# Kernel optimization log

Measured on AMD Instinct MI355X. Metric: run time of the kernel, lower is better.

## Reference

```python
import jax, jax.numpy as jnp
import numpy as np

D_MODEL, D_STATE, D_CONV, EXPAND = 1024, 16, 4, 2
D_INNER = D_MODEL * EXPAND
BATCH, SEQ = 2, 2048


def setup_inputs() -> dict:
    key = jax.random.key(0)
    ks = jax.random.split(key, 10)
    s = lambda d: 1.0 / np.sqrt(d)
    return {
        "x": jax.random.normal(ks[0], (BATCH, SEQ, D_MODEL), jnp.float32),
        "norm_w": jnp.ones((D_MODEL,), jnp.float32),
        "norm_b": jnp.zeros((D_MODEL,), jnp.float32),
        "W_in": jax.random.normal(ks[1], (2 * D_INNER, D_MODEL), jnp.float32) * s(D_MODEL),
        "conv_w": jax.random.normal(ks[2], (D_INNER, D_CONV), jnp.float32) * s(D_CONV),
        "conv_b": jnp.zeros((D_INNER,), jnp.float32),
        "W_dt": jax.random.normal(ks[3], (D_INNER, D_INNER), jnp.float32) * s(D_INNER),
        "b_dt": jnp.zeros((D_INNER,), jnp.float32),
        "W_B": jax.random.normal(ks[4], (D_STATE, D_INNER), jnp.float32) * s(D_INNER),
        "W_C": jax.random.normal(ks[5], (D_STATE, D_INNER), jnp.float32) * s(D_INNER),
        "D": jnp.ones((D_INNER,), jnp.float32),
        "A_log": jnp.broadcast_to(jnp.log(jnp.arange(1, D_STATE + 1, dtype=jnp.float32)), (D_INNER, D_STATE)),
        "W_out": jax.random.normal(ks[6], (D_MODEL, D_INNER), jnp.float32) * s(D_INNER),
    }


def _layernorm(x, w, b, eps=1e-5):
    mu = jnp.mean(x, axis=-1, keepdims=True)
    var = jnp.var(x, axis=-1, keepdims=True)
    return (x - mu) * jax.lax.rsqrt(var + eps) * w + b


def _causal_depthwise_conv(x, w, b):
    # x: [B, L, C], w: [C, K], b: [C]; torch Conv1d(padding=K-1) then slice [:L] == left-pad causal conv
    K = w.shape[1]
    xp = jnp.pad(x, ((0, 0), (K - 1, 0), (0, 0)))
    L = x.shape[1]
    out = b
    for k in range(K):  # small fixed K=4
        out = out + xp[:, k:k + L, :] * w[:, k]
    return out


def reference(x, norm_w, norm_b, W_in, conv_w, conv_b, W_dt, b_dt, W_B, W_C, D, A_log, W_out):
    residual = x
    xn = _layernorm(x, norm_w, norm_b)
    xz = jnp.einsum("bld,ed->ble", xn, W_in)            # [B,L,2*d_inner]
    x_part, z = jnp.split(xz, 2, axis=-1)
    x_conv = jax.nn.silu(_causal_depthwise_conv(x_part, conv_w, conv_b))  # [B,L,di]
    dt = jax.nn.softplus(jnp.einsum("bld,ed->ble", x_conv, W_dt) + b_dt)  # [B,L,di]
    Bm = jnp.einsum("bld,nd->bln", x_conv, W_B)         # [B,L,ds]
    Cm = jnp.einsum("bld,nd->bln", x_conv, W_C)         # [B,L,ds]
    A = -jnp.exp(A_log)                                  # [di,ds]

    def step(h, inp):
        dt_t, B_t, C_t, xc_t = inp                       # [B,di],[B,ds],[B,ds],[B,di]
        h = h * jnp.exp(A[None] * dt_t[:, :, None]) + xc_t[:, :, None] * B_t[:, None, :] * dt_t[:, :, None]
        y_t = jnp.sum(h * C_t[:, None, :], axis=-1)      # [B,di]
        return h, y_t

    h0 = jnp.zeros((x.shape[0], A.shape[0], A.shape[1]), x_conv.dtype)
    # scan over time: move L to leading axis
    xs = (jnp.swapaxes(dt, 0, 1), jnp.swapaxes(Bm, 0, 1), jnp.swapaxes(Cm, 0, 1), jnp.swapaxes(x_conv, 0, 1))
    _, y = jax.lax.scan(step, h0, xs)                    # y: [L,B,di]
    y = jnp.swapaxes(y, 0, 1)
    y = y + x_conv * D
    y = y * jax.nn.silu(z)
    return residual + jnp.einsum("ble,de->bld", y, W_out)
```

## Files before the change

### kernel.cpp

```cpp
#include <hip/hip_runtime.h>
#include <cstdint>
#include <cstddef>

#define D_MODEL 1024
#define D_INNER 2048
#define D_STATE 16
#define SEQ     2048
#define NROWS   4096

typedef short short4v __attribute__((ext_vector_type(4)));
typedef short short8v __attribute__((ext_vector_type(8)));
typedef float float4v __attribute__((ext_vector_type(4)));

__device__ __forceinline__ float bf2f(short u) {
  union { unsigned int i; float f; } v;
  v.i = ((unsigned int)(unsigned short)u) << 16;
  return v.f;
}
__device__ __forceinline__ short f2bf(float f) {
  union { float f; unsigned int i; } v; v.f = f;
  unsigned int r = v.i + 0x7FFFu + ((v.i >> 16) & 1u);
  return (short)(r >> 16);
}
__device__ __forceinline__ float lde(const void* p, size_t i, int f32) {
  return f32 ? ((const float*)p)[i] : bf2f(((const short*)p)[i]);
}
__device__ __forceinline__ void async16(short* lds, const short* g) {
  __builtin_amdgcn_global_load_lds(
      (const __attribute__((address_space(1))) unsigned int*)g,
      (__attribute__((address_space(3))) unsigned int*)lds, 16, 0, 0);
}

__global__ __launch_bounds__(64) void probe_kernel(const unsigned int* __restrict__ xw,
                                                   int* __restrict__ flag) {
  int cnt = 0;
  for (int i = threadIdx.x; i < 1024; i += 64) {
    unsigned e = (xw[i] >> 7) & 0xFFu;
    cnt += (e >= 100u && e <= 150u) ? 1 : 0;
  }
  #pragma unroll
  for (int o = 32; o >= 1; o >>= 1) cnt += __shfl_xor(cnt, o);
  if (threadIdx.x == 0) *flag = (cnt < 614) ? 1 : 0;
}

#define WIN_N  4194304u
#define WDT_N  4194304u
#define WBC_N  32768u
#define WPAD_N 196608u
#define WCAT_N (WDT_N + 2u*WBC_N + WPAD_N)
#define WOUT_N 2097152u
__global__ __launch_bounds__(256) void cvt_kernel(
    const void* __restrict__ Win, const void* __restrict__ Wdt,
    const void* __restrict__ WBp, const void* __restrict__ WCp,
    const void* __restrict__ Wout, short* __restrict__ dst,
    const int* __restrict__ flag) {
  const int f32 = *flag;
  const size_t i = ((size_t)blockIdx.x * 256 + threadIdx.x) * 8;
  const void* src = nullptr; size_t off = 0; bool zero = false;
  if (i < WIN_N) { src = Win; off = i; }
  else {
    size_t j = i - WIN_N;
    if (j < WDT_N) { src = Wdt; off = j; }
    else {
      j -= WDT_N;
      if (j < WBC_N) { src = WBp; off = j; }
      else {
        j -= WBC_N;
        if (j < WBC_N) { src = WCp; off = j; }
        else {
          j -= WBC_N;
          if (j < WPAD_N) zero = true;
          else { src = Wout; off = j - WPAD_N; }
        }
      }
    }
  }
  short8v o;
  if (zero) {
    #pragma unroll
    for (int j = 0; j < 8; ++j) o[j] = 0;
  } else if (f32) {
    const float* s = (const float*)src + off;
    #pragma unroll
    for (int j = 0; j < 8; ++j) o[j] = f2bf(s[j]);
  } else {
    o = *(const short8v*)((const short*)src + off);
  }
  *(short8v*)&dst[i] = o;
}

__global__ __launch_bounds__(256) void ln_kernel(
    const void* __restrict__ x, const void* __restrict__ w,
    const void* __restrict__ bb, short* __restrict__ xn,
    const int* __restrict__ flag) {
  const int f32 = *flag;
  const int row = blockIdx.x;
  const int tid = threadIdx.x;
  float v0, v1, v2, v3;
  if (f32) {
    float4v xv = ((const float4v*)((const float*)x + (size_t)row * D_MODEL))[tid];
    v0 = xv[0]; v1 = xv[1]; v2 = xv[2]; v3 = xv[3];
  } else {
    short4v xv = *(const short4v*)&((const short*)x)[(size_t)row * D_MODEL + tid * 4];
    v0 = bf2f(xv[0]); v1 = bf2f(xv[1]); v2 = bf2f(xv[2]); v3 = bf2f(xv[3]);
  }
  float s = v0 + v1 + v2 + v3;
  float q = v0*v0 + v1*v1 + v2*v2 + v3*v3;
  #pragma unroll
  for (int off = 32; off >= 1; off >>= 1) {
    s += __shfl_xor(s, off);
    q += __shfl_xor(q, off);
  }
  __shared__ float red[8];
  const int wid = tid >> 6;
  if ((tid & 63) == 0) { red[wid] = s; red[4 + wid] = q; }
  __syncthreads();
  s = red[0] + red[1] + red[2] + red[3];
  q = red[4] + red[5] + red[6] + red[7];
  const float mu = s * (1.f / 1024.f);
  const float var = q * (1.f / 1024.f) - mu * mu;
  const float rstd = rsqrtf(var + 1e-5f);
  short4v ov;
  #pragma unroll
  for (int j = 0; j < 4; ++j) {
    const float vj = (j == 0) ? v0 : (j == 1) ? v1 : (j == 2) ? v2 : v3;
    const float o = (vj - mu) * rstd * lde(w, tid * 4 + j, f32) + lde(bb, tid * 4 + j, f32);
    ov[j] = f2bf(o);
  }
  *(short4v*)&xn[(size_t)row * D_MODEL + tid * 4] = ov;
}

template <int MODE, int BM>
__global__ __launch_bounds__(2 * BM) void gemm_bt(
    const short* __restrict__ A, int lda, const short* __restrict__ B,
    void* __restrict__ Cv, int N, int K, const void* __restrict__ aux,
    float* __restrict__ Bmo, float* __restrict__ Cmo,
    const int* __restrict__ flag) {
  __shared__ __align__(16) short As0[BM * 32];
  __shared__ __align__(16) short As1[BM * 32];
  __shared__ __align__(16) short Bs0[128 * 32];
  __shared__ __align__(16) short Bs1[128 * 32];
  const int f32 = *flag;
  const int tid = threadIdx.x;
  const int bm = blockIdx.y * BM;
  const int bn = blockIdx.x << 7;
  const int wid = tid >> 6;
  const int lane = tid & 63;
  const int wm = (wid >> 1) << 6;
  const int wn = (wid & 1) << 6;

  float4v acc[4][4];
  #pragma unroll
  for (int i = 0; i < 4; ++i)
    #pragma unroll
    for (int j = 0; j < 4; ++j) acc[i][j] = (float4v){0.f, 0.f, 0.f, 0.f};

  const int srow = tid >> 2;
  const int scol = (((tid & 3) ^ ((tid >> 3) & 3)) << 3);
  const short* ga = A + (size_t)(bm + srow) * lda + scol;
  const short* gb = B + (size_t)(bn + srow) * K + scol;
  const size_t astep = (size_t)(BM / 2) * lda;
  const size_t bstep = (size_t)64 * K;

  const int fr = lane & 15;
  const int fq = (((lane >> 4) ^ ((lane >> 1) & 3)) << 3);

  constexpr int STAGE_DMAS = (BM == 256) ? 3 : 4;
  constexpr int VM_WAIT = 0x3FF0 | STAGE_DMAS;

#define STAGE(Ad, Bd, kk) do {                              \
    async16(&Ad[tid * 8], ga + (kk));                       \
    async16(&Ad[BM * 16 + tid * 8], ga + astep + (kk));     \
    if (BM == 256) {                                        \
      async16(&Bd[tid * 8], gb + (kk));                     \
    } else {                                                \
      async16(&Bd[tid * 8], gb + (kk));                     \
      async16(&Bd[2048 + tid * 8], gb + bstep + (kk));      \
    } } while (0)

  auto compute = [&](const short* Asrc, const short* Bsrc) {
    short8v af[4], bfv[4];
    #pragma unroll
    for (int i = 0; i < 4; ++i)
      af[i] = *(const short8v*)&Asrc[(wm + i * 16 + fr) * 32 + fq];
    #pragma unroll
    for (int j = 0; j < 4; ++j)
      bfv[j] = *(const short8v*)&Bsrc[(wn + j * 16 + fr) * 32 + fq];
    #pragma unroll
    for (int i = 0; i < 4; ++i)
      #pragma unroll
      for (int j = 0; j < 4; ++j)
        acc[i][j] = __builtin_amdgcn_mfma_f32_16x16x32_bf16(af[i], bfv[j], acc[i][j], 0, 0, 0);
  };

  const int nk = K >> 5;
  STAGE(As0, Bs0, 0);
  for (int k2 = 0; k2 < nk; k2 += 2) {
    STAGE(As1, Bs1, (k2 + 1) << 5);
    __builtin_amdgcn_s_waitcnt(VM_WAIT);
    __builtin_amdgcn_s_barrier();
    compute(As0, Bs0);
    __builtin_amdgcn_s_barrier();
    if (k2 + 2 < nk) {
      STAGE(As0, Bs0, (k2 + 2) << 5);
      __builtin_amdgcn_s_waitcnt(VM_WAIT);
    } else {
      __builtin_amdgcn_s_waitcnt(0x3FF0);
    }
    __builtin_amdgcn_s_barrier();
    compute(As1, Bs1);
    __builtin_amdgcn_s_barrier();
  }
#undef STAGE

  const int er = (lane >> 4) << 2;
  const int ec = lane & 15;
  #pragma unroll
  for (int i = 0; i < 4; ++i) {
    #pragma unroll
    for (int j = 0; j < 4; ++j) {
      const int gcol = bn + wn + j * 16 + ec;
      #pragma unroll
      for (int r = 0; r < 4; ++r) {
        const int grow = bm + wm + i * 16 + er + r;
        float v = acc[i][j][r];
        if (MODE == 1) {
          if (gcol < 2048) {
            v += lde(aux, gcol, f32);
            v = (v > 15.f) ? v : log1pf(__expf(v));
            ((short*)Cv)[(size_t)grow * 2048 + gcol] = f2bf(v);
          } else if (gcol < 2064) {
            Bmo[(size_t)grow * 16 + (gcol - 2048)] = v;
          } else if (gcol < 2080) {
            Cmo[(size_t)grow * 16 + (gcol - 2064)] = v;
          }
        } else {
          const size_t idx = (size_t)grow * N + gcol;
          if (MODE == 2) {
            v += lde(aux, idx, f32);
            if (f32) ((float*)Cv)[idx] = v;
            else     ((short*)Cv)[idx] = f2bf(v);
          } else {
            ((short*)Cv)[idx] = f2bf(v);
          }
        }
      }
    }
  }
}

__global__ __launch_bounds__(256) void bc_kernel(
    const short* __restrict__ xcv, const short* __restrict__ wbc,
    float* __restrict__ Bmo, float* __restrict__ Cmo) {
  const int tid = threadIdx.x;
  const int w = tid >> 6;
  const int lane = tid & 63;
  const int fr = lane & 15;
  const int hi = lane >> 4;
  const int r0 = blockIdx.x << 4;
  const short* ap  = xcv + (size_t)(r0 + fr) * 2048 + hi * 8;
  const short* b0p = wbc + (size_t)fr * 2048 + hi * 8;
  const short* b1p = wbc + (size_t)(16 + fr) * 2048 + hi * 8;
  float4v acc0 = (float4v){0.f, 0.f, 0.f, 0.f};
  float4v acc1 = (float4v){0.f, 0.f, 0.f, 0.f};
  #pragma unroll 4
  for (int k = w * 32; k < 2048; k += 128) {
    const short8v af  = *(const short8v*)(ap + k);
    const short8v bf0 = *(const short8v*)(b0p + k);
    const short8v bf1 = *(const short8v*)(b1p + k);
    acc0 = __builtin_amdgcn_mfma_f32_16x16x32_bf16(af, bf0, acc0, 0, 0, 0);
    acc1 = __builtin_amdgcn_mfma_f32_16x16x32_bf16(af, bf1, acc1, 0, 0, 0);
  }
  __shared__ float red[3][64][8];
  if (w) {
    #pragma unroll
    for (int r = 0; r < 4; ++r) {
      red[w - 1][lane][r]     = acc0[r];
      red[w - 1][lane][4 + r] = acc1[r];
    }
  }
  __syncthreads();
  if (w == 0) {
    #pragma unroll
    for (int c = 0; c < 3; ++c)
      #pragma unroll
      for (int r = 0; r < 4; ++r) {
        acc0[r] += red[c][lane][r];
        acc1[r] += red[c][lane][4 + r];
      }
    const int er = hi << 2;
    const int ec = fr;
    #pragma unroll
    for (int r = 0; r < 4; ++r) {
      Bmo[(size_t)(r0 + er + r) * 16 + ec] = acc0[r];
      Cmo[(size_t)(r0 + er + r) * 16 + ec] = acc1[r];
    }
  }
}

#define CONV_RPB 8
__global__ __launch_bounds__(256) void conv_silu(
    const short* __restrict__ xz, const void* __restrict__ cw,
    const void* __restrict__ cb, short* __restrict__ xc,
    const int* __restrict__ flag) {
  const int f32 = *flag;
  const int r0 = blockIdx.x * CONV_RPB;
  const int c0 = threadIdx.x << 3;
  const int t0 = r0 & (SEQ - 1);

  float wreg[32], bias[8];
  if (f32) {
    const float4v* wp = (const float4v*)((const float*)cw + (size_t)c0 * 4);
    #pragma unroll
    for (int q = 0; q < 8; ++q) {
      const float4v v = wp[q];
      #pragma unroll
      for (int k = 0; k < 4; ++k) wreg[q * 4 + k] = v[k];
    }
    const float4v* bp = (const float4v*)((const float*)cb + c0);
    const float4v b0 = bp[0], b1 = bp[1];
    #pragma unroll
    for (int j = 0; j < 4; ++j) { bias[j] = b0[j]; bias[4 + j] = b1[j]; }
  } else {
    const short8v* wp = (const short8v*)((const short*)cw + (size_t)c0 * 4);
    #pragma unroll
    for (int q = 0; q < 4; ++q) {
      const short8v v = wp[q];
      #pragma unroll
      for (int e = 0; e < 8; ++e) wreg[q * 8 + e] = bf2f(v[e]);
    }
    const short8v bv = *(const short8v*)((const short*)cb + c0);
    #pragma unroll
    for (int j = 0; j < 8; ++j) bias[j] = bf2f(bv[j]);
  }

  float xw[4][8];
  #pragma unroll
  for (int k = 0; k < 3; ++k) {
    if (t0 + k - 3 >= 0) {
      const short8v v = *(const short8v*)&xz[(size_t)(r0 + k - 3) * 4096 + c0];
      #pragma unroll
      for (int j = 0; j < 8; ++j) xw[k][j] = bf2f(v[j]);
    } else {
      #pragma unroll
      for (int j = 0; j < 8; ++j) xw[k][j] = 0.f;
    }
  }
  #pragma unroll
  for (int t = 0; t < CONV_RPB; ++t) {
    const int row = r0 + t;
    const short8v v = *(const short8v*)&xz[(size_t)row * 4096 + c0];
    #pragma unroll
    for (int j = 0; j < 8; ++j) xw[3][j] = bf2f(v[j]);
    short8v ov;
    #pragma unroll
    for (int j = 0; j < 8; ++j) {
      float a = bias[j];
      #pragma unroll
      for (int k = 0; k < 4; ++k) a += xw[k][j] * wreg[j * 4 + k];
      ov[j] = f2bf(a / (1.f + __expf(-a)));
    }
    *(short8v*)&xc[(size_t)row * D_INNER + c0] = ov;
    #pragma unroll
    for (int k = 0; k < 3; ++k)
      #pragma unroll
      for (int j = 0; j < 8; ++j) xw[k][j] = xw[k + 1][j];
  }
}

#define SCAN_CK 64
#define SCAN_ST 32
__global__ __launch_bounds__(1024, 4) void scan_kernel(
    const short* __restrict__ dtb, const short* __restrict__ xcv,
    const float* __restrict__ Bm, const float* __restrict__ Cm,
    short* __restrict__ xzb, const void* __restrict__ A_log,
    const void* __restrict__ Dv, const int* __restrict__ flag) {
  const int f32 = *flag;
  const int tid = threadIdx.x;
  const int dl = tid & 15;
  const int ck = tid >> 4;
  const int di = (blockIdx.x << 4) + dl;
  const int b = blockIdx.y;
  const int r0 = (b << 11) + ck * SCAN_ST;

  const short* dtp = dtb + (size_t)r0 * 2048 + di;
  const short* xcp = xcv + (size_t)r0 * 2048 + di;
  const float* bmp = Bm + (size_t)r0 * 16;
  const float* cmp = Cm + (size_t)r0 * 16;
  const short* zp = xzb + (size_t)r0 * 4096 + 2048 + di;
  short* yp = xzb + (size_t)r0 * 4096 + di;

  float Ac[16];
  #pragma unroll
  for (int s = 0; s < 16; ++s)
    Ac[s] = -__expf(lde(A_log, (size_t)di * 16 + s, f32));
  const float Dval = lde(Dv, di, f32);

  float h[16];
  #pragma unroll
  for (int s = 0; s < 16; ++s) h[s] = 0.f;
  float sdt = 0.f;

  #pragma unroll 2
  for (int t = 0; t < SCAN_ST; ++t) {
    const float dt = bf2f(dtp[(size_t)t * 2048]);
    const float xc = bf2f(xcp[(size_t)t * 2048]);
    const float4v b0 = *(const float4v*)&bmp[t * 16];
    const float4v b1 = *(const float4v*)&bmp[t * 16 + 4];
    const float4v b2 = *(const float4v*)&bmp[t * 16 + 8];
    const float4v b3 = *(const float4v*)&bmp[t * 16 + 12];
    sdt += dt;
    const float u = xc * dt;
    #pragma unroll
    for (int s = 0; s < 16; ++s) {
      const float bv = (s < 4) ? b0[s] : (s < 8) ? b1[s - 4] : (s < 12) ? b2[s - 8] : b3[s - 12];
      h[s] = h[s] * __expf(Ac[s] * dt) + u * bv;
    }
  }

  __shared__ float sdt_s[SCAN_CK][16];
  __shared__ float hc_s[SCAN_CK][16][17];
  sdt_s[ck][dl] = sdt;
  #pragma unroll
  for (int s = 0; s < 16; ++s) hc_s[ck][dl][s] = h[s];
  __syncthreads();
  if (tid < 256) {
    const int s = tid >> 4;
    const float Acs = -__expf(lde(A_log, (size_t)di * 16 + s, f32));
    float hs = 0.f;
    #pragma unroll 4
    for (int c = 0; c < SCAN_CK; ++c) {
      const float hend = hc_s[c][dl][s];
      hc_s[c][dl][s] = hs;
      hs = __expf(Acs * sdt_s[c][dl]) * hs + hend;
    }
  }
  __syncthreads();
  #pragma unroll
  for (int s = 0; s < 16; ++s) h[s] = hc_s[ck][dl][s];

  #pragma unroll 2
  for (int t = 0; t < SCAN_ST; ++t) {
    const float dt = bf2f(dtp[(size_t)t * 2048]);
    const float xc = bf2f(xcp[(size_t)t * 2048]);
    const float4v b0 = *(const float4v*)&bmp[t * 16];
    const float4v b1 = *(const float4v*)&bmp[t * 16 + 4];
    const float4v b2 = *(const float4v*)&bmp[t * 16 + 8];
    const float4v b3 = *(const float4v*)&bmp[t * 16 + 12];
    const float4v c0 = *(const float4v*)&cmp[t * 16];
    const float4v c1 = *(const float4v*)&cmp[t * 16 + 4];
    const float4v c2 = *(const float4v*)&cmp[t * 16 + 8];
    const float4v c3 = *(const float4v*)&cmp[t * 16 + 12];
    const float u = xc * dt;
    float p0 = 0.f, p1 = 0.f, p2 = 0.f, p3 = 0.f;
    #pragma unroll
    for (int s = 0; s < 4; ++s) {
      h[s]      = h[s]      * __expf(Ac[s]      * dt) + u * b0[s];
      h[s + 4]  = h[s + 4]  * __expf(Ac[s + 4]  * dt) + u * b1[s];
      h[s + 8]  = h[s + 8]  * __expf(Ac[s + 8]  * dt) + u * b2[s];
      h[s + 12] = h[s + 12] * __expf(Ac[s + 12] * dt) + u * b3[s];
      p0 += h[s] * c0[s];
      p1 += h[s + 4] * c1[s];
      p2 += h[s + 8] * c2[s];
      p3 += h[s + 12] * c3[s];
    }
    const float p = (p0 + p1) + (p2 + p3);
    const float z = bf2f(zp[(size_t)t * 4096]);
    const float sz = z / (1.f + __expf(-z));
    yp[(size_t)t * 4096] = f2bf((p + xc * Dval) * sz);
  }
}

extern "C" void kernel_launch(void* const* d_in, const int* in_sizes, int n_in,
                              void* d_out, int out_size, void* d_ws, size_t ws_size,
                              hipStream_t stream) {
  const void* x      = d_in[0];
  const void* norm_w = d_in[1];
  const void* norm_b = d_in[2];
  const void* W_in   = d_in[3];
  const void* conv_w = d_in[4];
  const void* conv_b = d_in[5];
  const void* W_dt   = d_in[6];
  const void* b_dt   = d_in[7];
  const void* W_B    = d_in[8];
  const void* W_C    = d_in[9];
  const void* Dv     = d_in[10];
  const void* A_log  = d_in[11];
  const void* W_out  = d_in[12];

  char* ws = (char*)d_ws;
  const size_t MB = (size_t)1 << 20;
  short* wcvt = (short*)(ws);
  short* wbuf = wcvt;
  short* wcat = wcvt + WIN_N;
  short* wout = wcvt + WIN_N + WCAT_N;
  int*   flag = (int*)(ws + 21 * MB - 256);
  short* xzb  = (short*)(ws + 21 * MB);
  short* xcv  = (short*)(ws + 53 * MB);
  short* xn   = (short*)(ws + 69 * MB);
  short* dtb  = (short*)(ws + 69 * MB);
  float* Bm   = (float*)(ws + 85 * MB);
  float* Cm   = Bm + (size_t)NROWS * 16;

  probe_kernel<<<1, 64, 0, stream>>>((const unsigned int*)x, flag);
  cvt_kernel<<<5248, 256, 0, stream>>>(W_in, W_dt, W_B, W_C, W_out, wcvt, flag);
  ln_kernel<<<NROWS, 256, 0, stream>>>(x, norm_w, norm_b, xn, flag);
  gemm_bt<0, 256><<<dim3(32, 16), 512, 0, stream>>>(xn, 1024, wbuf, xzb, 4096, 1024, nullptr, nullptr, nullptr, flag);
  conv_silu<<<NROWS / CONV_RPB, 256, 0, stream>>>(xzb, conv_w, conv_b, xcv, flag);
  gemm_bt<1, 256><<<dim3(16, 16), 512, 0, stream>>>(xcv, 2048, wcat, dtb, 2176, 2048, b_dt, nullptr, nullptr, flag);
  bc_kernel<<<256, 256, 0, stream>>>(xcv, wcat + (size_t)2048 * 2048, Bm, Cm);
  scan_kernel<<<dim3(128, 2), 1024, 0, stream>>>(dtb, xcv, Bm, Cm, xzb, A_log, Dv, flag);
  gemm_bt<2, 128><<<dim3(8, 32), 256, 0, stream>>>(xzb, 4096, wout, d_out, 1024, 2048, x, nullptr, nullptr, flag);
}
```

Measured before the change: 419.5 us.

## Transpose dt and x_conv to channel-major before scan for vectorized time loads

Adds a tiled LDS transpose kernel that rewrites x_conv and dt from row-major [rows, 2048] into channel-major [2048, 4096] buffers. The scan then reads 8 consecutive timesteps per channel with one 16-byte load instead of strided 2-byte loads. This removes scattered, poorly coalesced accesses in both scan passes. The cost is two extra kernel launches and an additional read and write of two 16 MB bf16 tensors.

```diff
diff --git a/kernel.cpp b/kernel.cpp
--- a/kernel.cpp
+++ b/kernel.cpp
@@ -368,10 +368,37 @@
   }
 }
 
+__global__ __launch_bounds__(256) void tr_kernel(
+    const short* __restrict__ in, short* __restrict__ out) {
+  __shared__ short ldsT[64][65];
+  const int c0 = blockIdx.x << 6;
+  const int r0 = blockIdx.y << 6;
+  const int tid = threadIdx.x;
+  const int rr = tid >> 4;
+  const int cc = (tid & 15) << 2;
+  #pragma unroll
+  for (int it = 0; it < 4; ++it) {
+    const int row = rr + (it << 4);
+    const short4v v = *(const short4v*)&in[(size_t)(r0 + row) * 2048 + c0 + cc];
+    #pragma unroll
+    for (int j = 0; j < 4; ++j) ldsT[cc + j][row] = v[j];
+  }
+  __syncthreads();
+  const int ch = tid >> 2;
+  const int rb = (tid & 3) << 4;
+  #pragma unroll
+  for (int k = 0; k < 4; ++k) {
+    short4v v;
+    #pragma unroll
+    for (int j = 0; j < 4; ++j) v[j] = ldsT[ch][rb + (k << 2) + j];
+    *(short4v*)&out[(size_t)(c0 + ch) * 4096 + r0 + rb + (k << 2)] = v;
+  }
+}
+
 #define SCAN_CK 64
 #define SCAN_ST 32
 __global__ __launch_bounds__(1024, 4) void scan_kernel(
-    const short* __restrict__ dtb, const short* __restrict__ xcv,
+    const short* __restrict__ dtt, const short* __restrict__ xct,
     const float* __restrict__ Bm, const float* __restrict__ Cm,
     short* __restrict__ xzb, const void* __restrict__ A_log,
     const void* __restrict__ Dv, const int* __restrict__ flag) {
@@ -383,8 +410,8 @@
   const int b = blockIdx.y;
   const int r0 = (b << 11) + ck * SCAN_ST;
 
-  const short* dtp = dtb + (size_t)r0 * 2048 + di;
-  const short* xcp = xcv + (size_t)r0 * 2048 + di;
+  const short* dtp = dtt + (size_t)di * 4096 + r0;
+  const short* xcp = xct + (size_t)di * 4096 + r0;
   const float* bmp = Bm + (size_t)r0 * 16;
   const float* cmp = Cm + (size_t)r0 * 16;
   const short* zp = xzb + (size_t)r0 * 4096 + 2048 + di;
@@ -401,20 +428,27 @@
   for (int s = 0; s < 16; ++s) h[s] = 0.f;
   float sdt = 0.f;
 
-  #pragma unroll 2
-  for (int t = 0; t < SCAN_ST; ++t) {
-    const float dt = bf2f(dtp[(size_t)t * 2048]);
-    const float xc = bf2f(xcp[(size_t)t * 2048]);
-    const float4v b0 = *(const float4v*)&bmp[t * 16];
-    const float4v b1 = *(const float4v*)&bmp[t * 16 + 4];
-    const float4v b2 = *(const float4v*)&bmp[t * 16 + 8];
-    const float4v b3 = *(const float4v*)&bmp[t * 16 + 12];
-    sdt += dt;
-    const float u = xc * dt;
-    #pragma unroll
-    for (int s = 0; s < 16; ++s) {
-      const float bv = (s < 4) ? b0[s] : (s < 8) ? b1[s - 4] : (s < 12) ? b2[s - 8] : b3[s - 12];
-      h[s] = h[s] * __expf(Ac[s] * dt) + u * bv;
+  for (int t8 = 0; t8 < SCAN_ST / 8; ++t8) {
+    const short8v d8 = *(const short8v*)(dtp + t8 * 8);
+    const short8v x8 = *(const short8v*)(xcp + t8 * 8);
+    #pragma unroll
+    for (int tt = 0; tt < 8; ++tt) {
+      const int t = t8 * 8 + tt;
+      const float dt = bf2f(d8[tt]);
+      const float xc = bf2f(x8[tt]);
+      const float4v b0 = *(const float4v*)&bmp[t * 16];
+      const float4v b1 = *(const float4v*)&bmp[t * 16 + 4];
+      const float4v b2 = *(const float4v*)&bmp[t * 16 + 8];
+      const float4v b3 = *(const float4v*)&bmp[t * 16 + 12];
+      sdt += dt;
+      const float u = xc * dt;
+      #pragma unroll
+      for (int s = 0; s < 4; ++s) {
+        h[s]      = h[s]      * __expf(Ac[s]      * dt) + u * b0[s];
+        h[s + 4]  = h[s + 4]  * __expf(Ac[s + 4]  * dt) + u * b1[s];
+        h[s + 8]  = h[s + 8]  * __expf(Ac[s + 8]  * dt) + u * b2[s];
+        h[s + 12] = h[s + 12] * __expf(Ac[s + 12] * dt) + u * b3[s];
+      }
     }
   }
 
@@ -439,35 +473,40 @@
   #pragma unroll
   for (int s = 0; s < 16; ++s) h[s] = hc_s[ck][dl][s];
 
-  #pragma unroll 2
-  for (int t = 0; t < SCAN_ST; ++t) {
-    const float dt = bf2f(dtp[(size_t)t * 2048]);
-    const float xc = bf2f(xcp[(size_t)t * 2048]);
-    const float4v b0 = *(const float4v*)&bmp[t * 16];
-    const float4v b1 = *(const float4v*)&bmp[t * 16 + 4];
-    const float4v b2 = *(const float4v*)&bmp[t * 16 + 8];
-    const float4v b3 = *(const float4v*)&bmp[t * 16 + 12];
-    const float4v c0 = *(const float4v*)&cmp[t * 16];
-    const float4v c1 = *(const float4v*)&cmp[t * 16 + 4];
-    const float4v c2 = *(const float4v*)&cmp[t * 16 + 8];
-    const float4v c3 = *(const float4v*)&cmp[t * 16 + 12];
-    const float u = xc * dt;
-    float p0 = 0.f, p1 = 0.f, p2 = 0.f, p3 = 0.f;
-    #pragma unroll
-    for (int s = 0; s < 4; ++s) {
-      h[s]      = h[s]      * __expf(Ac[s]      * dt) + u * b0[s];
-      h[s + 4]  = h[s + 4]  * __expf(Ac[s + 4]  * dt) + u * b1[s];
-      h[s + 8]  = h[s + 8]  * __expf(Ac[s + 8]  * dt) + u * b2[s];
-      h[s + 12] = h[s + 12] * __expf(Ac[s + 12] * dt) + u * b3[s];
-      p0 += h[s] * c0[s];
-      p1 += h[s + 4] * c1[s];
-      p2 += h[s + 8] * c2[s];
-      p3 += h[s + 12] * c3[s];
-    }
-    const float p = (p0 + p1) + (p2 + p3);
-    const float z = bf2f(zp[(size_t)t * 4096]);
-    const float sz = z / (1.f + __expf(-z));
-    yp[(size_t)t * 4096] = f2bf((p + xc * Dval) * sz);
+  for (int t8 = 0; t8 < SCAN_ST / 8; ++t8) {
+    const short8v d8 = *(const short8v*)(dtp + t8 * 8);
+    const short8v x8 = *(const short8v*)(xcp + t8 * 8);
+    #pragma unroll
+    for (int tt = 0; tt < 8; ++tt) {
+      const int t = t8 * 8 + tt;
+      const float dt = bf2f(d8[tt]);
+      const float xc = bf2f(x8[tt]);
+      const float4v b0 = *(const float4v*)&bmp[t * 16];
+      const float4v b1 = *(const float4v*)&bmp[t * 16 + 4];
+      const float4v b2 = *(const float4v*)&bmp[t * 16 + 8];
+      const float4v b3 = *(const float4v*)&bmp[t * 16 + 12];
+      const float4v c0 = *(const float4v*)&cmp[t * 16];
+      const float4v c1 = *(const float4v*)&cmp[t * 16 + 4];
+      const float4v c2 = *(const float4v*)&cmp[t * 16 + 8];
+      const float4v c3 = *(const float4v*)&cmp[t * 16 + 12];
+      const float u = xc * dt;
+      float p0 = 0.f, p1 = 0.f, p2 = 0.f, p3 = 0.f;
+      #pragma unroll
+      for (int s = 0; s < 4; ++s) {
+        h[s]      = h[s]      * __expf(Ac[s]      * dt) + u * b0[s];
+        h[s + 4]  = h[s + 4]  * __expf(Ac[s + 4]  * dt) + u * b1[s];
+        h[s + 8]  = h[s + 8]  * __expf(Ac[s + 8]  * dt) + u * b2[s];
+        h[s + 12] = h[s + 12] * __expf(Ac[s + 12] * dt) + u * b3[s];
+        p0 += h[s] * c0[s];
+        p1 += h[s + 4] * c1[s];
+        p2 += h[s + 8] * c2[s];
+        p3 += h[s + 12] * c3[s];
+      }
+      const float p = (p0 + p1) + (p2 + p3);
+      const float z = bf2f(zp[(size_t)t * 4096]);
+      const float sz = z / (1.f + __expf(-z));
+      yp[(size_t)t * 4096] = f2bf((p + xc * Dval) * sz);
+    }
   }
 }
 
@@ -497,10 +536,12 @@
   int*   flag = (int*)(ws + 21 * MB - 256);
   short* xzb  = (short*)(ws + 21 * MB);
   short* xcv  = (short*)(ws + 53 * MB);
+  short* dtt  = (short*)(ws + 53 * MB);
   short* xn   = (short*)(ws + 69 * MB);
   short* dtb  = (short*)(ws + 69 * MB);
   float* Bm   = (float*)(ws + 85 * MB);
   float* Cm   = Bm + (size_t)NROWS * 16;
+  short* xct  = (short*)(ws + 86 * MB);
 
   probe_kernel<<<1, 64, 0, stream>>>((const unsigned int*)x, flag);
   cvt_kernel<<<5248, 256, 0, stream>>>(W_in, W_dt, W_B, W_C, W_out, wcvt, flag);
@@ -509,6 +550,8 @@
   conv_silu<<<NROWS / CONV_RPB, 256, 0, stream>>>(xzb, conv_w, conv_b, xcv, flag);
   gemm_bt<1, 256><<<dim3(16, 16), 512, 0, stream>>>(xcv, 2048, wcat, dtb, 2176, 2048, b_dt, nullptr, nullptr, flag);
   bc_kernel<<<256, 256, 0, stream>>>(xcv, wcat + (size_t)2048 * 2048, Bm, Cm);
-  scan_kernel<<<dim3(128, 2), 1024, 0, stream>>>(dtb, xcv, Bm, Cm, xzb, A_log, Dv, flag);
+  tr_kernel<<<dim3(32, 64), 256, 0, stream>>>(xcv, xct);
+  tr_kernel<<<dim3(32, 64), 256, 0, stream>>>(dtb, dtt);
+  scan_kernel<<<dim3(128, 2), 1024, 0, stream>>>(dtt, xct, Bm, Cm, xzb, A_log, Dv, flag);
   gemm_bt<2, 128><<<dim3(8, 32), 256, 0, stream>>>(xzb, 4096, wout, d_out, 1024, 2048, x, nullptr, nullptr, flag);
 }
```

After: 431.4 us. 2.8% more time.
